# Optimization experiments

Measured on AMD Instinct MI355X. Metric: run time of the kernel, lower is better.

Reference implementation:

```python
import jax, jax.numpy as jnp
import numpy as np

NS, NV = 32, 8                      # scalar / vector multiplicities (32x0e + 8x1o)
N_NODES, N_EDGES = 16384, 131072
NEF, HID = 128, 128                 # edge feature dim, MLP hidden
WN = NS*NS + NV*NS + NS*NV + NV*NV  # 1600 tensor-product weights per edge
D = NS + 3*NV                       # 56 node feature dim
INV_SQRT3 = 1.0/np.sqrt(3.0)        # CG coeff for 1o x 1o -> 0e
PATH_NORM = 1.0/np.sqrt(NS + NV)    # fan-in normalization per output irrep
EPS = 1e-5


def setup_inputs() -> dict:
    key = jax.random.key(0)
    ks = jax.random.split(key, 10)
    node_attr = jax.random.normal(ks[0], (N_NODES, D), jnp.float32)
    edge_index = jax.random.randint(ks[1], (2, N_EDGES), 0, N_NODES, dtype=jnp.int64)
    edge_attr = jax.random.normal(ks[2], (N_EDGES, NEF), jnp.float32)
    edge_sh = jax.random.normal(ks[3], (N_EDGES, 4), jnp.float32)
    W1 = jax.random.normal(ks[4], (NEF, HID), jnp.float32) / np.sqrt(NEF)
    b1 = jnp.zeros((HID,), jnp.float32)
    W2 = jax.random.normal(ks[5], (HID, WN), jnp.float32) / np.sqrt(HID)
    b2 = jnp.zeros((WN,), jnp.float32)
    bn_gamma = jnp.ones((NS + NV,), jnp.float32)   # per-irrep scale (scalars then vectors)
    bn_beta = jnp.zeros((NS,), jnp.float32)        # bias only on scalar irreps
    return dict(node_attr=node_attr, edge_attr=edge_attr, edge_sh=edge_sh,
                W1=W1, b1=b1, W2=W2, b2=b2, bn_gamma=bn_gamma, bn_beta=bn_beta,
                edge_index=edge_index)


def reference(node_attr, edge_attr, edge_sh, W1, b1, W2, b2, bn_gamma, bn_beta, edge_index):
    edge_src, edge_dst = edge_index[0], edge_index[1]

    # per-edge tensor-product weights from edge MLP (dropout=0, eval mode)
    w = jax.nn.relu(edge_attr @ W1 + b1) @ W2 + b2            # [E, WN]
    o0 = NS*NS; o1 = o0 + NV*NS; o2 = o1 + NS*NV
    w_ss = w[:, :o0].reshape(-1, NS, NS)   # 0e x 0e -> 0e
    w_vs = w[:, o0:o1].reshape(-1, NV, NS) # 1o x 1o -> 0e
    w_sv = w[:, o1:o2].reshape(-1, NS, NV) # 0e x 1o -> 1o
    w_vv = w[:, o2:].reshape(-1, NV, NV)   # 1o x 0e -> 1o

    # gather node features onto edges
    x = node_attr[edge_dst]                # [E, D]
    xs = x[:, :NS]                         # [E, NS]
    xv = x[:, NS:].reshape(-1, NV, 3)      # [E, NV, 3]
    ss = edge_sh[:, 0]                     # [E]
    sv = edge_sh[:, 1:4]                   # [E, 3]

    # CG tensor product with per-edge fully-connected weights
    dot_vv = jnp.einsum('eim,em->ei', xv, sv) * INV_SQRT3
    out_s = (jnp.einsum('eij,ei->ej', w_ss, xs) * ss[:, None]
             + jnp.einsum('eij,ei->ej', w_vs, dot_vv)) * PATH_NORM          # [E, NS]
    out_v = (jnp.einsum('eij,ei->ej', w_sv, xs)[:, :, None] * sv[:, None, :]
             + jnp.einsum('eij,eim->ejm', w_vv, xv) * ss[:, None, None]) * PATH_NORM  # [E, NV, 3]
    tp = jnp.concatenate([out_s, out_v.reshape(-1, 3*NV)], axis=-1)         # [E, D]

    # scatter-mean to source nodes
    sums = jax.ops.segment_sum(tp, edge_src, num_segments=N_NODES)
    cnt = jax.ops.segment_sum(jnp.ones((tp.shape[0], 1), tp.dtype), edge_src,
                              num_segments=N_NODES)
    out = sums / jnp.maximum(cnt, 1.0)

    # residual (in/out irreps identical -> zero padding is a no-op)
    out = out + node_attr

    # equivariant batch norm (training-mode batch statistics)
    s = out[:, :NS]
    v = out[:, NS:].reshape(-1, NV, 3)
    s = (s - s.mean(0)) / jnp.sqrt(s.var(0) + EPS) * bn_gamma[:NS] + bn_beta
    vn2 = (v * v).sum(-1).mean(0)                               # [NV] mean squared norm
    v = v / jnp.sqrt(vn2 + EPS)[None, :, None] * bn_gamma[NS:][None, :, None]
    return jnp.concatenate([s, v.reshape(-1, 3*NV)], axis=-1)
```

## Files before the change

### kernel.cpp

```cpp
#include <hip/hip_runtime.h>

typedef short short8 __attribute__((ext_vector_type(8)));
typedef unsigned short us4 __attribute__((ext_vector_type(4)));
typedef float floatx4 __attribute__((ext_vector_type(4)));
typedef unsigned short u16;

#define NN 16384
#define NE 131072
#define NEF_ 128
#define DD 56
#define INV_SQRT3F 0.57735026918962576f
#define PATH_NORMF 0.15811388300841897f

__device__ __forceinline__ float bf2f(u16 u) {
    union { unsigned int i; float f; } v; v.i = ((unsigned int)u) << 16; return v.f;
}
__device__ __forceinline__ u16 f2bf(float f) {
    union { float f; unsigned int i; } v; v.f = f;
    unsigned int r = v.i + 0x7fffu + ((v.i >> 16) & 1u);
    return (u16)(r >> 16);
}

__global__ __launch_bounds__(256) void prep(const float* __restrict__ W1,
                                            const float* __restrict__ W2,
                                            u16* __restrict__ W1T,
                                            u16* __restrict__ W2T,
                                            const int* __restrict__ eidx,
                                            int* __restrict__ deg) {
    int b = blockIdx.x;
    if (b < 864) {
        int i = b * 256 + threadIdx.x;
        if (i < 16384) {
            int n = i >> 7, k = i & 127;
            W1T[i] = f2bf(W1[k * 128 + n]);
        } else {
            int j = i - 16384;
            int n = j >> 7, k = j & 127;
            W2T[j] = f2bf(W2[k * 1600 + n]);
        }
    } else {
        int e = (b - 864) * 256 + threadIdx.x;
        atomicAdd(&deg[eidx[e]], 1);
    }
}

__global__ __launch_bounds__(1024) void deg_scan(const int* __restrict__ deg,
                                                 int* __restrict__ row_start,
                                                 int* __restrict__ cursor) {
    __shared__ int part[1024];
    const int t = threadIdx.x;
    const int base = t * 16;
    int loc[16];
    int s = 0;
    #pragma unroll
    for (int i = 0; i < 16; i++) { loc[i] = s; s += deg[base + i]; }
    part[t] = s;
    __syncthreads();
    for (int off = 1; off < 1024; off <<= 1) {
        int v = (t >= off) ? part[t - off] : 0;
        __syncthreads();
        part[t] += v;
        __syncthreads();
    }
    int pre = (t == 0) ? 0 : part[t - 1];
    #pragma unroll
    for (int i = 0; i < 16; i++) {
        int v = pre + loc[i];
        row_start[base + i] = v;
        cursor[base + i] = v;
    }
    if (t == 1023) row_start[16384] = pre + s;
}

__global__ __launch_bounds__(256) void edge_scatter(const int* __restrict__ eidx,
                                                    int* __restrict__ cursor,
                                                    int* __restrict__ edge_order) {
    int e = blockIdx.x * 256 + threadIdx.x;
    int p = atomicAdd(&cursor[eidx[e]], 1);
    edge_order[p] = e;
}

__global__ __launch_bounds__(256, 2) void tpconv(
    const float* __restrict__ node_attr, const float* __restrict__ edge_attr,
    const float* __restrict__ edge_sh, const u16* __restrict__ W1T,
    const float* __restrict__ b1, const u16* __restrict__ W2T,
    const float* __restrict__ b2, const int* __restrict__ eidx,
    float* __restrict__ tp)
{
    __shared__ __align__(16) char smem[49920];
    u16*   sA  = (u16*)smem;
    u16*   sB  = (u16*)(smem + 17408);
    u16*   sF  = (u16*)(smem + 34816);
    float* b2s = (float*)(smem + 43520);
    float* Ssc  = (float*)smem;
    float* Svec = (float*)(smem + 16896);

    const int t = threadIdx.x;
    const int lane = t & 63;
    const int wv = t >> 6;
    const int m = lane & 15;
    const int q = lane >> 4;
    const int Rb = (wv >> 1) * 32;
    const int Cb = (wv & 1) * 32;
    const int e0 = blockIdx.x * 64;
    const int str = t >> 4;
    const int stc = (t & 15) * 8;

    short8 pre[4];
    #pragma unroll
    for (int ii = 0; ii < 4; ii++)
        pre[ii] = *(const short8*)&W2T[(size_t)(str + 16 * ii) * 128 + stc];

    for (int i = t; i < 1600; i += 256) b2s[i] = b2[i];

    #pragma unroll
    for (int ii = 0; ii < 8; ii++) {
        int cid = t + 256 * ii;
        int r = cid >> 5, s = cid & 31;
        const float* src = &edge_attr[(size_t)(e0 + r) * NEF_ + s * 4];
        us4 o;
        o.x = f2bf(src[0]); o.y = f2bf(src[1]); o.z = f2bf(src[2]); o.w = f2bf(src[3]);
        *(us4*)&sA[r * 136 + s * 4] = o;
    }
    if (t < 64) {
        int nd = eidx[NE + e0 + t];
        const float* na = node_attr + (size_t)nd * DD;
        const float* sh = edge_sh + (size_t)(e0 + t) * 4;
        float ss = sh[0], s0 = sh[1], s1 = sh[2], s2 = sh[3];
        #pragma unroll
        for (int i = 0; i < 32; i++) sF[i * 64 + t] = f2bf(na[i]);
        #pragma unroll
        for (int i = 0; i < 8; i++) {
            float d = (na[32+i*3]*s0 + na[33+i*3]*s1 + na[34+i*3]*s2) * INV_SQRT3F;
            sF[(32 + i) * 64 + t] = f2bf(d);
        }
        #pragma unroll
        for (int i = 0; i < 24; i++) sF[(40 + i) * 64 + t] = f2bf(na[32 + i]);
        sF[64 * 64 + t] = f2bf(ss);
        sF[65 * 64 + t] = f2bf(s0);
        sF[66 * 64 + t] = f2bf(s1);
        sF[67 * 64 + t] = f2bf(s2);
    }
    __syncthreads();

    floatx4 hacc[2][2][2];
    #pragma unroll
    for (int cc = 0; cc < 2; cc++) {
        #pragma unroll
        for (int ii = 0; ii < 4; ii++)
            *(short8*)&sB[(str + 16 * ii) * 136 + stc] =
                *(const short8*)&W1T[(size_t)(cc * 64 + str + 16 * ii) * 128 + stc];
        __syncthreads();
        #pragma unroll
        for (int rt = 0; rt < 2; rt++)
            #pragma unroll
            for (int ct = 0; ct < 2; ct++) {
                float bv = b1[cc * 64 + Cb + ct * 16 + m];
                hacc[cc][rt][ct] = (floatx4){bv, bv, bv, bv};
            }
        #pragma unroll
        for (int k0 = 0; k0 < 128; k0 += 32) {
            short8 a0 = *(const short8*)&sA[(Rb      + m) * 136 + k0 + q * 8];
            short8 a1 = *(const short8*)&sA[(Rb + 16 + m) * 136 + k0 + q * 8];
            short8 bA = *(const short8*)&sB[(Cb      + m) * 136 + k0 + q * 8];
            short8 bB = *(const short8*)&sB[(Cb + 16 + m) * 136 + k0 + q * 8];
            hacc[cc][0][0] = __builtin_amdgcn_mfma_f32_16x16x32_bf16(a0, bA, hacc[cc][0][0], 0, 0, 0);
            hacc[cc][0][1] = __builtin_amdgcn_mfma_f32_16x16x32_bf16(a0, bB, hacc[cc][0][1], 0, 0, 0);
            hacc[cc][1][0] = __builtin_amdgcn_mfma_f32_16x16x32_bf16(a1, bA, hacc[cc][1][0], 0, 0, 0);
            hacc[cc][1][1] = __builtin_amdgcn_mfma_f32_16x16x32_bf16(a1, bB, hacc[cc][1][1], 0, 0, 0);
        }
        __syncthreads();
    }
    #pragma unroll
    for (int cc = 0; cc < 2; cc++)
      #pragma unroll
      for (int rt = 0; rt < 2; rt++)
        #pragma unroll
        for (int ct = 0; ct < 2; ct++)
          #pragma unroll
          for (int r = 0; r < 4; r++) {
              int e   = Rb + rt * 16 + q * 4 + r;
              int col = cc * 64 + Cb + ct * 16 + m;
              float v = hacc[cc][rt][ct][r];
              sA[e * 136 + col] = f2bf(v > 0.f ? v : 0.f);
          }
    __syncthreads();

    short8 hc[4][4];
    #pragma unroll
    for (int et = 0; et < 4; et++)
        #pragma unroll
        for (int kk = 0; kk < 4; kk++)
            hc[et][kk] = *(const short8*)&sA[(et * 16 + m) * 136 + kk * 32 + q * 8];

    float ssc[4], svc[4][3];
    #pragma unroll
    for (int et = 0; et < 4; et++) {
        ssc[et] = bf2f(sF[64 * 64 + et * 16 + m]);
        svc[et][0] = bf2f(sF[65 * 64 + et * 16 + m]);
        svc[et][1] = bf2f(sF[66 * 64 + et * 16 + m]);
        svc[et][2] = bf2f(sF[67 * 64 + et * 16 + m]);
    }

    #pragma unroll
    for (int ii = 0; ii < 4; ii++)
        *(short8*)&sB[(str + 16 * ii) * 136 + stc] = pre[ii];
    #pragma unroll
    for (int ii = 0; ii < 4; ii++)
        pre[ii] = *(const short8*)&W2T[(size_t)(64 + str + 16 * ii) * 128 + stc];
    __syncthreads();

    float tps[4][4];
    float tpv[4][4][3];
    #pragma unroll
    for (int et = 0; et < 4; et++)
        #pragma unroll
        for (int r = 0; r < 4; r++) {
            tps[et][r] = 0.f;
            tpv[et][r][0] = 0.f; tpv[et][r][1] = 0.f; tpv[et][r][2] = 0.f;
        }

    for (int c = 0; c < 25; c++) {
        floatx4 bias = *(const floatx4*)&b2s[c * 64 + wv * 16 + q * 4];
        floatx4 acc[4];
        #pragma unroll
        for (int et = 0; et < 4; et++) acc[et] = bias;
        #pragma unroll
        for (int kk = 0; kk < 4; kk++) {
            short8 a = *(const short8*)&sB[(wv * 16 + m) * 136 + kk * 32 + q * 8];
            acc[0] = __builtin_amdgcn_mfma_f32_16x16x32_bf16(a, hc[0][kk], acc[0], 0, 0, 0);
            acc[1] = __builtin_amdgcn_mfma_f32_16x16x32_bf16(a, hc[1][kk], acc[1], 0, 0, 0);
            acc[2] = __builtin_amdgcn_mfma_f32_16x16x32_bf16(a, hc[2][kk], acc[2], 0, 0, 0);
            acc[3] = __builtin_amdgcn_mfma_f32_16x16x32_bf16(a, hc[3][kk], acc[3], 0, 0, 0);
        }

        if (c < 16) {
            const int i = 2 * c + (wv >> 1);
            #pragma unroll
            for (int et = 0; et < 4; et++) {
                float f = bf2f(sF[i * 64 + et * 16 + m]) * ssc[et];
                #pragma unroll
                for (int r = 0; r < 4; r++) tps[et][r] += acc[et][r] * f;
            }
        } else if (c < 20) {
            const int i = 2 * (c - 16) + (wv >> 1);
            #pragma unroll
            for (int et = 0; et < 4; et++) {
                float f = bf2f(sF[(32 + i) * 64 + et * 16 + m]);
                #pragma unroll
                for (int r = 0; r < 4; r++) tps[et][r] += acc[et][r] * f;
            }
        } else if (c < 24) {
            const int i = 8 * (c - 20) + wv * 2 + (q >> 1);
            #pragma unroll
            for (int et = 0; et < 4; et++) {
                float f = bf2f(sF[i * 64 + et * 16 + m]);
                #pragma unroll
                for (int r = 0; r < 4; r++) {
                    float t0 = acc[et][r] * f;
                    tpv[et][r][0] += t0 * svc[et][0];
                    tpv[et][r][1] += t0 * svc[et][1];
                    tpv[et][r][2] += t0 * svc[et][2];
                }
            }
        } else {
            const int i = wv * 2 + (q >> 1);
            #pragma unroll
            for (int et = 0; et < 4; et++) {
                float x0 = bf2f(sF[(40 + 3 * i + 0) * 64 + et * 16 + m]) * ssc[et];
                float x1 = bf2f(sF[(40 + 3 * i + 1) * 64 + et * 16 + m]) * ssc[et];
                float x2 = bf2f(sF[(40 + 3 * i + 2) * 64 + et * 16 + m]) * ssc[et];
                #pragma unroll
                for (int r = 0; r < 4; r++) {
                    tpv[et][r][0] += acc[et][r] * x0;
                    tpv[et][r][1] += acc[et][r] * x1;
                    tpv[et][r][2] += acc[et][r] * x2;
                }
            }
        }

        __syncthreads();
        if (c < 24) {
            #pragma unroll
            for (int ii = 0; ii < 4; ii++)
                *(short8*)&sB[(str + 16 * ii) * 136 + stc] = pre[ii];
            if (c < 23) {
                #pragma unroll
                for (int ii = 0; ii < 4; ii++)
                    pre[ii] = *(const short8*)&W2T[(size_t)((c + 2) * 64 + str + 16 * ii) * 128 + stc];
            }
        }
        __syncthreads();
    }

    #pragma unroll
    for (int et = 0; et < 4; et++)
        #pragma unroll
        for (int r = 0; r < 4; r++)
            Ssc[(wv >> 1) * 2112 + (et * 16 + m) * 33 + (wv & 1) * 16 + q * 4 + r] = tps[et][r];
    #pragma unroll
    for (int et = 0; et < 4; et++)
        #pragma unroll
        for (int r = 0; r < 4; r++)
            #pragma unroll
            for (int mm = 0; mm < 3; mm++) {
                float v = tpv[et][r][mm];
                v += __shfl_xor(v, 32, 64);
                if (q < 2)
                    Svec[wv * 1600 + (et * 16 + m) * 25 + ((q & 1) * 4 + r) * 3 + mm] = v;
            }
    __syncthreads();

    for (int idx = t; idx < 3584; idx += 256) {
        int e = idx / 56, d = idx - e * 56;
        float v;
        if (d < 32) {
            v = Ssc[e * 33 + d] + Ssc[2112 + e * 33 + d];
        } else {
            int dd = d - 32;
            v = Svec[e * 25 + dd] + Svec[1600 + e * 25 + dd]
              + Svec[3200 + e * 25 + dd] + Svec[4800 + e * 25 + dd];
        }
        tp[(size_t)(e0 + e) * DD + d] = v * PATH_NORMF;
    }
}

__global__ __launch_bounds__(256) void gather_finalize(
    const float* __restrict__ tp, const int* __restrict__ row_start,
    const int* __restrict__ edge_order, const float* __restrict__ node_attr,
    float* __restrict__ ybuf)
{
    const int wv = threadIdx.x >> 6, lane = threadIdx.x & 63;
    const int n = blockIdx.x * 4 + wv;
    const int beg = row_start[n], end = row_start[n + 1];
    if (lane < 56) {
        float acc = 0.f;
        int e_next = (beg < end) ? edge_order[beg] : 0;
        for (int p = beg; p < end; p++) {
            int e = e_next;
            if (p + 1 < end) e_next = edge_order[p + 1];
            acc += tp[(size_t)e * DD + lane];
        }
        float inv = 1.f / fmaxf((float)(end - beg), 1.f);
        float y = acc * inv + node_attr[(size_t)n * DD + lane];
        ybuf[(size_t)n * DD + lane] = y;
    }
}

__global__ __launch_bounds__(256) void bn_stats(const float* __restrict__ ybuf,
                                                float* __restrict__ stats)
{
    __shared__ float red[256];
    const int d = blockIdx.x;
    const int t = threadIdx.x;
    float a = 0.f;
    if (d < 32) {
        for (int n = t; n < NN; n += 256) a += ybuf[(size_t)n * DD + d];
    } else if (d < 64) {
        int dd = d - 32;
        for (int n = t; n < NN; n += 256) {
            float v = ybuf[(size_t)n * DD + dd];
            a += v * v;
        }
    } else {
        int jv = d - 64;
        for (int n = t; n < NN; n += 256) {
            float v0 = ybuf[(size_t)n * DD + 32 + jv * 3];
            float v1 = ybuf[(size_t)n * DD + 33 + jv * 3];
            float v2 = ybuf[(size_t)n * DD + 34 + jv * 3];
            a += v0 * v0 + v1 * v1 + v2 * v2;
        }
    }
    red[t] = a;
    __syncthreads();
    for (int off = 128; off > 0; off >>= 1) {
        if (t < off) red[t] += red[t + off];
        __syncthreads();
    }
    if (t == 0) stats[d] = red[0] * (1.f / 16384.f);
}

__global__ __launch_bounds__(256) void bn_apply(
    const float* __restrict__ ybuf, const float* __restrict__ stats,
    const float* __restrict__ gamma, const float* __restrict__ beta,
    float* __restrict__ out)
{
    const int i = blockIdx.x * 256 + threadIdx.x;
    const int n = i / 56;
    const int d = i - n * 56;
    float y = ybuf[i];
    float o;
    if (d < 32) {
        float mn  = stats[d];
        float var = stats[32 + d] - mn * mn;
        o = (y - mn) * rsqrtf(var + 1e-5f) * gamma[d] + beta[d];
    } else {
        int jv = (d - 32) / 3;
        o = y * rsqrtf(stats[64 + jv] + 1e-5f) * gamma[32 + jv];
    }
    out[i] = o;
}

extern "C" void kernel_launch(void* const* d_in, const int* in_sizes, int n_in,
                              void* d_out, int out_size, void* d_ws, size_t ws_size,
                              hipStream_t stream)
{
    const float* node_attr = (const float*)d_in[0];
    const float* edge_attr = (const float*)d_in[1];
    const float* edge_sh   = (const float*)d_in[2];
    const float* W1        = (const float*)d_in[3];
    const float* b1        = (const float*)d_in[4];
    const float* W2        = (const float*)d_in[5];
    const float* b2        = (const float*)d_in[6];
    const float* gamma     = (const float*)d_in[7];
    const float* beta      = (const float*)d_in[8];
    const int*   eidx      = (const int*)d_in[9];

    char* ws = (char*)d_ws;
    u16*   W1T        = (u16*)(ws);
    u16*   W2T        = (u16*)(ws + 32768);
    int*   deg        = (int*)(ws + 442368);
    int*   row_start  = (int*)(ws + 507904);
    int*   cursor     = (int*)(ws + 573696);
    int*   edge_order = (int*)(ws + 639232);
    float* stats      = (float*)(ws + 1163520);
    float* tp         = (float*)(ws + 1164032);
    float* ybuf       = (float*)(ws + 30524160);

    (void)hipMemsetAsync(deg, 0, 65536, stream);
    hipLaunchKernelGGL(prep,            dim3(1376), dim3(256),  0, stream,
                       W1, W2, W1T, W2T, eidx, deg);
    hipLaunchKernelGGL(deg_scan,        dim3(1),    dim3(1024), 0, stream, deg, row_start, cursor);
    hipLaunchKernelGGL(edge_scatter,    dim3(512),  dim3(256),  0, stream, eidx, cursor, edge_order);
    hipLaunchKernelGGL(tpconv,          dim3(2048), dim3(256),  0, stream,
                       node_attr, edge_attr, edge_sh, W1T, b1, W2T, b2, eidx, tp);
    hipLaunchKernelGGL(gather_finalize, dim3(4096), dim3(256),  0, stream,
                       tp, row_start, edge_order, node_attr, ybuf);
    hipLaunchKernelGGL(bn_stats,        dim3(72),   dim3(256),  0, stream, ybuf, stats);
    hipLaunchKernelGGL(bn_apply,        dim3(3584), dim3(256),  0, stream,
                       ybuf, stats, gamma, beta, (float*)d_out);
}
```

Measured before the change: 285.6 us.

## Load W2 MFMA fragments directly to registers and fuse BN stats into gather

In the tensor-product kernel, each wave now loads its W2 A-fragments straight from global memory into a double-buffered register set. This replaces staging them through shared memory with two block barriers per chunk, and the chunk loop is fully unrolled. Separately, gather_finalize now writes per-block partial sums for the batch-norm statistics, and a small reduce kernel replaces the strided column scan over ybuf. The cost is more global traffic per wave for W2 (each wave loads its own slice, with no sharing through LDS), higher register pressure from the unroll, and an extra partial buffer in the workspace.

Result: slower. 332.3 us (+16.4%).

```diff
diff --git a/kernel.cpp b/kernel.cpp
--- a/kernel.cpp
+++ b/kernel.cpp
@@ -106,10 +106,12 @@
     const int str = t >> 4;
     const int stc = (t & 15) * 8;
 
-    short8 pre[4];
-    #pragma unroll
-    for (int ii = 0; ii < 4; ii++)
-        pre[ii] = *(const short8*)&W2T[(size_t)(str + 16 * ii) * 128 + stc];
+    const u16* wfrag = W2T + (size_t)(wv * 16 + m) * 128 + q * 8;
+    short8 fa[2][4];
+    #pragma unroll
+    for (int kk = 0; kk < 4; kk++) fa[0][kk] = *(const short8*)(wfrag + kk * 32);
+    #pragma unroll
+    for (int kk = 0; kk < 4; kk++) fa[1][kk] = *(const short8*)(wfrag + 8192 + kk * 32);
 
     for (int i = t; i < 1600; i += 256) b2s[i] = b2[i];
 
@@ -202,14 +204,6 @@
         svc[et][2] = bf2f(sF[67 * 64 + et * 16 + m]);
     }
 
-    #pragma unroll
-    for (int ii = 0; ii < 4; ii++)
-        *(short8*)&sB[(str + 16 * ii) * 136 + stc] = pre[ii];
-    #pragma unroll
-    for (int ii = 0; ii < 4; ii++)
-        pre[ii] = *(const short8*)&W2T[(size_t)(64 + str + 16 * ii) * 128 + stc];
-    __syncthreads();
-
     float tps[4][4];
     float tpv[4][4][3];
     #pragma unroll
@@ -220,6 +214,7 @@
             tpv[et][r][0] = 0.f; tpv[et][r][1] = 0.f; tpv[et][r][2] = 0.f;
         }
 
+    #pragma unroll
     for (int c = 0; c < 25; c++) {
         floatx4 bias = *(const floatx4*)&b2s[c * 64 + wv * 16 + q * 4];
         floatx4 acc[4];
@@ -227,11 +222,16 @@
         for (int et = 0; et < 4; et++) acc[et] = bias;
         #pragma unroll
         for (int kk = 0; kk < 4; kk++) {
-            short8 a = *(const short8*)&sB[(wv * 16 + m) * 136 + kk * 32 + q * 8];
+            short8 a = fa[c & 1][kk];
             acc[0] = __builtin_amdgcn_mfma_f32_16x16x32_bf16(a, hc[0][kk], acc[0], 0, 0, 0);
             acc[1] = __builtin_amdgcn_mfma_f32_16x16x32_bf16(a, hc[1][kk], acc[1], 0, 0, 0);
             acc[2] = __builtin_amdgcn_mfma_f32_16x16x32_bf16(a, hc[2][kk], acc[2], 0, 0, 0);
             acc[3] = __builtin_amdgcn_mfma_f32_16x16x32_bf16(a, hc[3][kk], acc[3], 0, 0, 0);
+        }
+        if (c < 23) {
+            #pragma unroll
+            for (int kk = 0; kk < 4; kk++)
+                fa[c & 1][kk] = *(const short8*)(wfrag + (size_t)(c + 2) * 8192 + kk * 32);
         }
 
         if (c < 16) {
@@ -278,20 +278,8 @@
                 }
             }
         }
-
-        __syncthreads();
-        if (c < 24) {
-            #pragma unroll
-            for (int ii = 0; ii < 4; ii++)
-                *(short8*)&sB[(str + 16 * ii) * 136 + stc] = pre[ii];
-            if (c < 23) {
-                #pragma unroll
-                for (int ii = 0; ii < 4; ii++)
-                    pre[ii] = *(const short8*)&W2T[(size_t)((c + 2) * 64 + str + 16 * ii) * 128 + stc];
-            }
-        }
-        __syncthreads();
-    }
+    }
+    __syncthreads();
 
     #pragma unroll
     for (int et = 0; et < 4; et++)
@@ -328,8 +316,9 @@
 __global__ __launch_bounds__(256) void gather_finalize(
     const float* __restrict__ tp, const int* __restrict__ row_start,
     const int* __restrict__ edge_order, const float* __restrict__ node_attr,
-    float* __restrict__ ybuf)
+    float* __restrict__ ybuf, float* __restrict__ partial)
 {
+    __shared__ float ps[4][72];
     const int wv = threadIdx.x >> 6, lane = threadIdx.x & 63;
     const int n = blockIdx.x * 4 + wv;
     const int beg = row_start[n], end = row_start[n + 1];
@@ -344,33 +333,31 @@
         float inv = 1.f / fmaxf((float)(end - beg), 1.f);
         float y = acc * inv + node_attr[(size_t)n * DD + lane];
         ybuf[(size_t)n * DD + lane] = y;
-    }
-}
-
-__global__ __launch_bounds__(256) void bn_stats(const float* __restrict__ ybuf,
-                                                float* __restrict__ stats)
+        if (lane < 32) {
+            ps[wv][lane] = y;
+            ps[wv][32 + lane] = y * y;
+        } else {
+            float vv = y * y;
+            float v1 = __shfl_down(vv, 1, 64);
+            float v2 = __shfl_down(vv, 2, 64);
+            int l3 = lane - 32;
+            if (l3 % 3 == 0) ps[wv][64 + l3 / 3] = vv + v1 + v2;
+        }
+    }
+    __syncthreads();
+    const int t = threadIdx.x;
+    if (t < 72)
+        partial[(size_t)blockIdx.x * 72 + t] = ps[0][t] + ps[1][t] + ps[2][t] + ps[3][t];
+}
+
+__global__ __launch_bounds__(256) void bn_reduce(const float* __restrict__ partial,
+                                                 float* __restrict__ stats)
 {
     __shared__ float red[256];
     const int d = blockIdx.x;
     const int t = threadIdx.x;
     float a = 0.f;
-    if (d < 32) {
-        for (int n = t; n < NN; n += 256) a += ybuf[(size_t)n * DD + d];
-    } else if (d < 64) {
-        int dd = d - 32;
-        for (int n = t; n < NN; n += 256) {
-            float v = ybuf[(size_t)n * DD + dd];
-            a += v * v;
-        }
-    } else {
-        int jv = d - 64;
-        for (int n = t; n < NN; n += 256) {
-            float v0 = ybuf[(size_t)n * DD + 32 + jv * 3];
-            float v1 = ybuf[(size_t)n * DD + 33 + jv * 3];
-            float v2 = ybuf[(size_t)n * DD + 34 + jv * 3];
-            a += v0 * v0 + v1 * v1 + v2 * v2;
-        }
-    }
+    for (int i = t; i < 4096; i += 256) a += partial[(size_t)i * 72 + d];
     red[t] = a;
     __syncthreads();
     for (int off = 128; off > 0; off >>= 1) {
@@ -424,8 +411,9 @@
     int*   cursor     = (int*)(ws + 573696);
     int*   edge_order = (int*)(ws + 639232);
     float* stats      = (float*)(ws + 1163520);
-    float* tp         = (float*)(ws + 1164032);
-    float* ybuf       = (float*)(ws + 30524160);
+    float* partial    = (float*)(ws + 1164032);
+    float* tp         = (float*)(ws + 2343680);
+    float* ybuf       = (float*)(ws + 31703808);
 
     (void)hipMemsetAsync(deg, 0, 65536, stream);
     hipLaunchKernelGGL(prep,            dim3(1376), dim3(256),  0, stream,
@@ -435,8 +423,8 @@
     hipLaunchKernelGGL(tpconv,          dim3(2048), dim3(256),  0, stream,
                        node_attr, edge_attr, edge_sh, W1T, b1, W2T, b2, eidx, tp);
     hipLaunchKernelGGL(gather_finalize, dim3(4096), dim3(256),  0, stream,
-                       tp, row_start, edge_order, node_attr, ybuf);
-    hipLaunchKernelGGL(bn_stats,        dim3(72),   dim3(256),  0, stream, ybuf, stats);
+                       tp, row_start, edge_order, node_attr, ybuf, partial);
+    hipLaunchKernelGGL(bn_reduce,       dim3(72),   dim3(256),  0, stream, partial, stats);
     hipLaunchKernelGGL(bn_apply,        dim3(3584), dim3(256),  0, stream,
                        ybuf, stats, gamma, beta, (float*)d_out);
 }
```
